# Optimization experiments

Measured on AMD Instinct MI355X. Metric: run time of the kernel, lower is better.

## Reference

```python
import jax, jax.numpy as jnp
import numpy as np

B = 1024
IN_H, IN_W = 128, 128
KH, KW = 10, 10
SH, SW = 5, 5
PH, PW = 2, 2
HP, WP = IN_H + 2 * PH, IN_W + 2 * PW          # padded dims: 132, 132
NKH = (IN_H - KH + 2 * PH) // SH + 1            # 25
NKW = (IN_W - KW + 2 * PW) // SW + 1            # 25
NK = NKH * NKW                                  # 625


def _build_weight_matrix(kernel_weights):
    """kernel_weights: [NK, KH, KW] -> sparse-structured dense [HP*WP, NK].
    Faithful to LocallyConnected2dV2._create_weight_matrix, vectorized."""
    i = jnp.arange(NK)
    start_i = (i // NKW) * SH                   # [NK]
    start_j = (i % NKW) * SW                    # [NK]
    # flat row index for each (kernel, k, l) tap in padded image
    rows = ((start_i[:, None, None] + jnp.arange(KH)[None, :, None]) * WP
            + start_j[:, None, None] + jnp.arange(KW)[None, None, :])  # [NK,KH,KW]
    rows = rows.reshape(NK, KH * KW)
    cols = i[:, None]                           # [NK,1] broadcasts over taps
    W = jnp.zeros((HP * WP, NK), dtype=kernel_weights.dtype)
    return W.at[rows, cols].set(kernel_weights.reshape(NK, KH * KW))


def setup_inputs() -> dict:
    key = jax.random.key(0)
    kx, kw, kb = jax.random.split(key, 3)
    x = jax.random.normal(kx, (B, IN_H, IN_W), dtype=jnp.float32)
    kernel_weights = jax.random.normal(kw, (NK, KH, KW), dtype=jnp.float32)
    W = _build_weight_matrix(kernel_weights)    # [HP*WP, NK]
    bias = jax.random.normal(kb, (NKH, NKW), dtype=jnp.float32)
    return {"x": x, "W": W, "bias": bias}


def reference(x, W, bias):
    # zero-pad spatial dims, flatten, dense GEMM against sparse-structured W
    xp = jnp.pad(x, ((0, 0), (PH, PH), (PW, PW)))          # [B,HP,WP]
    xf = xp.reshape(x.shape[0], HP * WP)                   # [B,HP*WP]
    out = xf @ W                                           # [B,NK]
    out = out.reshape(x.shape[0], NKH, NKW)
    return out + bias
```

## Files before the change

kernel.cpp:

```cpp
#include <hip/hip_runtime.h>

typedef _Float16 f16x2 __attribute__((ext_vector_type(2)));
typedef __fp16  fp16x2 __attribute__((ext_vector_type(2)));

constexpr int NKW  = 25, NK = 625;
constexpr int WPADR = 132;
constexpr int WPT   = 160;
constexpr int RST   = 35;
constexpr int RTOT  = 132;
constexpr int NCHUNK = 5;

union U2H { unsigned int u; f16x2 h; fp16x2 p; };

__global__ void gather_wp(const float* __restrict__ W, _Float16* __restrict__ wgpT) {
    int t = blockIdx.x * 256 + threadIdx.x;
    if (t >= NK * WPT) return;
    int k = t / WPT, p = t % WPT;
    int di = p >> 4, s = p & 15;
    int ki = k / NKW, kj = k % NKW;
    int o = (5 * kj + 2) & 3;
    int j = s - o;
    float val = 0.f;
    if (j >= 0 && j < 10)
        val = W[(size_t)((ki * 5 + di) * WPADR + kj * 5 + j) * NK + k];
    wgpT[((size_t)(p >> 3) * NK + k) * 8 + (p & 7)] = (_Float16)val;
}

__device__ __forceinline__ float dot2acc(unsigned int a, unsigned int b, float c) {
    U2H ua, ub; ua.u = a; ub.u = b;
#if __has_builtin(__builtin_amdgcn_fdot2)
    return __builtin_amdgcn_fdot2(ua.h, ub.h, c, false);
#else
    return c + (float)ua.h.x * (float)ub.h.x + (float)ua.h.y * (float)ub.h.y;
#endif
}

template <bool USE_WG>
__global__ __launch_bounds__(256, 4)
void lc2d_img(const float* __restrict__ x, const _Float16* __restrict__ wgpT,
              const float* __restrict__ Wfull,
              const float* __restrict__ bias, float* __restrict__ out) {
    __shared__ uint2 xs[RTOT * RST];

    const int b    = blockIdx.x;
    const int tid  = threadIdx.x;
    const int lane = tid & 63;
    const int pairbase = (tid >> 6) * 32 + (lane & 31);
    const int half = lane >> 5;
    const int di0  = half * 5;

    const float* xb = x + ((size_t)b << 14);
#pragma unroll 1
    for (int bt = 0; bt < 3; ++bt) {
        float4 tmp[6];
#pragma unroll
        for (int u = 0; u < 6; ++u) {
            const int i = tid + (bt * 6 + u) * 256;
            tmp[u] = make_float4(0.f, 0.f, 0.f, 0.f);
            if (i < RTOT * 32) {
                const int idx = i >> 5, q = i & 31, r = idx - 2;
                if (r >= 0 && r < 128)
                    tmp[u] = *reinterpret_cast<const float4*>(xb + (r << 7) + (q << 2));
            }
        }
#pragma unroll
        for (int u = 0; u < 6; ++u) {
            const int i = tid + (bt * 6 + u) * 256;
            if (i < RTOT * 32) {
                const int idx = i >> 5, q = (i & 31) + 1;
                U2H u0, u1;
                u0.p = __builtin_amdgcn_cvt_pkrtz(tmp[u].x, tmp[u].y);
                u1.p = __builtin_amdgcn_cvt_pkrtz(tmp[u].z, tmp[u].w);
                xs[idx * RST + q] = make_uint2(u0.u, u1.u);
            }
        }
    }
    for (int i = tid; i < 2 * RTOT; i += 256)
        xs[(i >> 1) * RST + (i & 1) * 33] = make_uint2(0u, 0u);

    auto load_w = [&](int c, uint4* w, float& bv) {
        const int pr = c * 128 + pairbase;
        if (pr >= NK) return;
        if constexpr (USE_WG) {
            const uint4* wt4 = reinterpret_cast<const uint4*>(wgpT);
#pragma unroll
            for (int j = 0; j < 10; ++j) w[j] = wt4[(size_t)(half * 10 + j) * NK + pr];
        } else {
            const int ki = pr / 25, kj = pr - ki * 25;
            const int o = (5 * kj + 2) & 3;
#pragma unroll
            for (int j = 0; j < 10; ++j) {
                const int di = di0 + (j >> 1), pb = (j & 1) * 8;
                unsigned int uu[4];
#pragma unroll
                for (int m = 0; m < 4; ++m) {
                    float f0 = 0.f, f1 = 0.f;
                    const int j0 = pb + 2 * m - o, j1 = pb + 2 * m + 1 - o;
                    const size_t rowb = (size_t)((ki * 5 + di) * WPADR + kj * 5);
                    if (j0 >= 0 && j0 < 10) f0 = Wfull[(rowb + j0) * NK + pr];
                    if (j1 >= 0 && j1 < 10) f1 = Wfull[(rowb + j1) * NK + pr];
                    U2H u; u.p = __builtin_amdgcn_cvt_pkrtz(f0, f1);
                    uu[m] = u.u;
                }
                w[j] = make_uint4(uu[0], uu[1], uu[2], uu[3]);
            }
        }
        if (half == 0) bv = bias[pr];
    };

    auto compute_chunk = [&](int c, const uint4* w, float bv) {
        const int pr = c * 128 + pairbase;
        float acc0 = 0.f, acc1 = 0.f;
        if (pr < NK) {
            const int ki = pr / 25, kj = pr - ki * 25;
            const uint2* base = xs + (5 * ki + di0) * RST + ((5 * kj + 2) >> 2);
#pragma unroll
            for (int d = 0; d < 5; ++d) {
                const uint2* rowp = base + d * RST;
                const uint2 a0 = rowp[0], a1 = rowp[1], a2 = rowp[2], a3 = rowp[3];
                const uint4 wA = w[2 * d], wB = w[2 * d + 1];
                acc0 = dot2acc(a0.x, wA.x, acc0);
                acc1 = dot2acc(a0.y, wA.y, acc1);
                acc0 = dot2acc(a1.x, wA.z, acc0);
                acc1 = dot2acc(a1.y, wA.w, acc1);
                acc0 = dot2acc(a2.x, wB.x, acc0);
                acc1 = dot2acc(a2.y, wB.y, acc1);
                acc0 = dot2acc(a3.x, wB.z, acc0);
                acc1 = dot2acc(a3.y, wB.w, acc1);
            }
        }
        float acc = acc0 + acc1;
        float other = __shfl_xor(acc, 32, 64);
        if (pr < NK && half == 0)
            out[(size_t)b * NK + pr] = acc + other + bv;
    };

    uint4 wA[10], wB[10];
    float bA = 0.f, bB = 0.f;
    load_w(0, wA, bA);
    load_w(1, wB, bB);
    __syncthreads();
    compute_chunk(0, wA, bA); load_w(2, wA, bA);
    compute_chunk(1, wB, bB); load_w(3, wB, bB);
    compute_chunk(2, wA, bA); load_w(4, wA, bA);
    compute_chunk(3, wB, bB);
    compute_chunk(4, wA, bA);
}

extern "C" void kernel_launch(void* const* d_in, const int* in_sizes, int n_in,
                              void* d_out, int out_size, void* d_ws, size_t ws_size,
                              hipStream_t stream) {
    const float* x    = (const float*)d_in[0];
    const float* W    = (const float*)d_in[1];
    const float* bias = (const float*)d_in[2];
    float* out = (float*)d_out;

    const dim3 grid(1024);
    if (ws_size >= (size_t)NK * WPT * sizeof(_Float16)) {
        _Float16* wgpT = (_Float16*)d_ws;
        gather_wp<<<(NK * WPT + 255) / 256, 256, 0, stream>>>(W, wgpT);
        lc2d_img<true><<<grid, 256, 0, stream>>>(x, wgpT, W, bias, out);
    } else {
        lc2d_img<false><<<grid, 256, 0, stream>>>(x, nullptr, W, bias, out);
    }
}
```

Measured before the change: 126.7 us.

## Split image staging to overlap later row loads with early chunk compute

```diff
diff --git a/kernel.cpp b/kernel.cpp
--- a/kernel.cpp
+++ b/kernel.cpp
@@ -8,7 +8,7 @@
 constexpr int WPT   = 160;
 constexpr int RST   = 35;
 constexpr int RTOT  = 132;
-constexpr int NCHUNK = 5;
+constexpr int NITEM = RTOT * 32;
 
 union U2H { unsigned int u; f16x2 h; fp16x2 p; };
 
@@ -48,43 +48,43 @@
     const int pairbase = (tid >> 6) * 32 + (lane & 31);
     const int half = lane >> 5;
     const int di0  = half * 5;
+    const float* xb = x + ((size_t)b << 14);
 
-    const float* xb = x + ((size_t)b << 14);
-#pragma unroll 1
-    for (int bt = 0; bt < 3; ++bt) {
-        float4 tmp[6];
+    auto stage_load4 = [&](int u0, float4* tmp) {
 #pragma unroll
-        for (int u = 0; u < 6; ++u) {
-            const int i = tid + (bt * 6 + u) * 256;
+        for (int u = 0; u < 4; ++u) {
+            const int i = tid + (u0 + u) * 256;
             tmp[u] = make_float4(0.f, 0.f, 0.f, 0.f);
-            if (i < RTOT * 32) {
+            if (i < NITEM) {
                 const int idx = i >> 5, q = i & 31, r = idx - 2;
                 if (r >= 0 && r < 128)
                     tmp[u] = *reinterpret_cast<const float4*>(xb + (r << 7) + (q << 2));
             }
         }
+    };
+    auto stage_write4 = [&](int u0, const float4* tmp) {
 #pragma unroll
-        for (int u = 0; u < 6; ++u) {
-            const int i = tid + (bt * 6 + u) * 256;
-            if (i < RTOT * 32) {
+        for (int u = 0; u < 4; ++u) {
+            const int i = tid + (u0 + u) * 256;
+            if (i < NITEM) {
                 const int idx = i >> 5, q = (i & 31) + 1;
-                U2H u0, u1;
-                u0.p = __builtin_amdgcn_cvt_pkrtz(tmp[u].x, tmp[u].y);
-                u1.p = __builtin_amdgcn_cvt_pkrtz(tmp[u].z, tmp[u].w);
-                xs[idx * RST + q] = make_uint2(u0.u, u1.u);
+                U2H u0h, u1h;
+                u0h.p = __builtin_amdgcn_cvt_pkrtz(tmp[u].x, tmp[u].y);
+                u1h.p = __builtin_amdgcn_cvt_pkrtz(tmp[u].z, tmp[u].w);
+                xs[idx * RST + q] = make_uint2(u0h.u, u1h.u);
             }
         }
-    }
-    for (int i = tid; i < 2 * RTOT; i += 256)
-        xs[(i >> 1) * RST + (i & 1) * 33] = make_uint2(0u, 0u);
+    };
 
-    auto load_w = [&](int c, uint4* w, float& bv) {
+    uint4 wq[10];
+    float bv = 0.f;
+    auto load_w = [&](int c) {
         const int pr = c * 128 + pairbase;
         if (pr >= NK) return;
         if constexpr (USE_WG) {
             const uint4* wt4 = reinterpret_cast<const uint4*>(wgpT);
 #pragma unroll
-            for (int j = 0; j < 10; ++j) w[j] = wt4[(size_t)(half * 10 + j) * NK + pr];
+            for (int j = 0; j < 10; ++j) wq[j] = wt4[(size_t)(half * 10 + j) * NK + pr];
         } else {
             const int ki = pr / 25, kj = pr - ki * 25;
             const int o = (5 * kj + 2) & 3;
@@ -102,13 +102,13 @@
                     U2H u; u.p = __builtin_amdgcn_cvt_pkrtz(f0, f1);
                     uu[m] = u.u;
                 }
-                w[j] = make_uint4(uu[0], uu[1], uu[2], uu[3]);
+                wq[j] = make_uint4(uu[0], uu[1], uu[2], uu[3]);
             }
         }
         if (half == 0) bv = bias[pr];
     };
 
-    auto compute_chunk = [&](int c, const uint4* w, float bv) {
+    auto compute_chunk = [&](int c) {
         const int pr = c * 128 + pairbase;
         float acc0 = 0.f, acc1 = 0.f;
         if (pr < NK) {
@@ -118,7 +118,7 @@
             for (int d = 0; d < 5; ++d) {
                 const uint2* rowp = base + d * RST;
                 const uint2 a0 = rowp[0], a1 = rowp[1], a2 = rowp[2], a3 = rowp[3];
-                const uint4 wA = w[2 * d], wB = w[2 * d + 1];
+                const uint4 wA = wq[2 * d], wB = wq[2 * d + 1];
                 acc0 = dot2acc(a0.x, wA.x, acc0);
                 acc1 = dot2acc(a0.y, wA.y, acc1);
                 acc0 = dot2acc(a1.x, wA.z, acc0);
@@ -135,16 +135,49 @@
             out[(size_t)b * NK + pr] = acc + other + bv;
     };
 
-    uint4 wA[10], wB[10];
-    float bA = 0.f, bB = 0.f;
-    load_w(0, wA, bA);
-    load_w(1, wB, bB);
+    for (int i = tid; i < 2 * RTOT; i += 256)
+        xs[(i >> 1) * RST + (i & 1) * 33] = make_uint2(0u, 0u);
+
+    {
+        float4 t[4];
+        stage_load4(0, t);  stage_write4(0, t);
+        stage_load4(4, t);  stage_write4(4, t);
+    }
+    load_w(0);
     __syncthreads();
-    compute_chunk(0, wA, bA); load_w(2, wA, bA);
-    compute_chunk(1, wB, bB); load_w(3, wB, bB);
-    compute_chunk(2, wA, bA); load_w(4, wA, bA);
-    compute_chunk(3, wB, bB);
-    compute_chunk(4, wA, bA);
+
+    {
+        float4 t[4];
+        stage_load4(8, t);
+        compute_chunk(0);
+        load_w(1);
+        stage_write4(8, t);
+        stage_load4(12, t);
+        compute_chunk(1);
+        load_w(2);
+        stage_write4(12, t);
+        float4 t1 = make_float4(0.f, 0.f, 0.f, 0.f);
+        const int i16 = tid + 4096;
+        if (i16 < NITEM) {
+            const int idx = i16 >> 5, q = i16 & 31, r = idx - 2;
+            if (r >= 0 && r < 128)
+                t1 = *reinterpret_cast<const float4*>(xb + (r << 7) + (q << 2));
+        }
+        if (i16 < NITEM) {
+            const int idx = i16 >> 5, q = (i16 & 31) + 1;
+            U2H u0h, u1h;
+            u0h.p = __builtin_amdgcn_cvt_pkrtz(t1.x, t1.y);
+            u1h.p = __builtin_amdgcn_cvt_pkrtz(t1.z, t1.w);
+            xs[idx * RST + q] = make_uint2(u0h.u, u1h.u);
+        }
+    }
+    __syncthreads();
+
+    compute_chunk(2);
+    load_w(3);
+    compute_chunk(3);
+    load_w(4);
+    compute_chunk(4);
 }
 
 extern "C" void kernel_launch(void* const* d_in, const int* in_sizes, int n_in,
```

Measured after the change: 126.6 us. Within noise of the previous version (-0.1%).
